# Kernel optimization log

Hardware: AMD Instinct MI355X
Metric: run time of the kernel (lower is better)

Reference implementation:

```python
import jax, jax.numpy as jnp
import numpy as np

G, NPG, MAXN = 1024, 40, 51   # graphs, nodes/graph, dense pad size
EPG = 80                       # edges per graph
N, E = G * NPG, G * EPG
D_IN, D_OUT, D_EDGE = 64, 32, 16


def _lin(key, fan_in, shape):
    b = 1.0 / np.sqrt(fan_in)
    return jax.random.uniform(key, shape, jnp.float32, -b, b)


def setup_inputs() -> dict:
    key = jax.random.key(0)
    ks = jax.random.split(key, 24)
    node_features = jax.random.randint(ks[0], (N, 9), 0, 128)
    edge_features = jax.random.randint(ks[1], (E, 3), 0, 8)
    offs = jnp.repeat(jnp.arange(G) * NPG, EPG)
    src = jax.random.randint(ks[2], (E,), 0, NPG) + offs
    dst = jax.random.randint(ks[3], (E,), 0, NPG) + offs
    edge_index = jnp.stack([src, dst])
    batch = jnp.repeat(jnp.arange(G), NPG)
    inp = dict(node_features=node_features, edge_features=edge_features,
               edge_index=edge_index, batch=batch)
    # OGB-style encoders: one embedding table per feature column, summed
    inp['atom_emb'] = jax.random.normal(ks[4], (9, 128, D_IN), jnp.float32) * 0.1
    inp['bond_emb'] = jax.random.normal(ks[5], (3, 8, D_EDGE), jnp.float32) * 0.1
    # edge-conditioned weight MLP: 16 -> 1024 -> 256 -> 64*32 (no bias)
    inp['gW1'] = _lin(ks[6], 16, (16, 1024))
    inp['gW2'] = _lin(ks[7], 1024, (1024, 256))
    inp['gW3'] = _lin(ks[8], 256, (256, D_IN * D_OUT))
    # NNConv root weight + bias
    inp['root'] = _lin(ks[9], D_IN, (D_IN, D_OUT))
    inp['conv_bias'] = jnp.zeros((D_OUT,), jnp.float32)
    # readout MLP: 51*32 -> 256 -> 128 -> 32 -> 8 -> 1
    dims = [MAXN * D_OUT, 256, 128, 32, 8, 1]
    for i in range(5):
        inp[f'mW{i+1}'] = _lin(ks[10 + 2 * i], dims[i], (dims[i], dims[i + 1]))
        inp[f'mb{i+1}'] = _lin(ks[11 + 2 * i], dims[i], (dims[i + 1],))
    return inp


def reference(node_features, edge_features, edge_index, batch,
              atom_emb, bond_emb, gW1, gW2, gW3, root, conv_bias,
              mW1, mb1, mW2, mb2, mW3, mb3, mW4, mb4, mW5, mb5):
    # encoders: sum of per-column embeddings
    x = jnp.sum(atom_emb[jnp.arange(9), node_features], axis=1)      # [N,64]
    e = jnp.sum(bond_emb[jnp.arange(3), edge_features], axis=1)      # [E,16]
    # per-edge weight matrix via MLP
    h = jax.nn.relu(e @ gW1)
    h = jax.nn.relu(h @ gW2)
    w = (h @ gW3).reshape(-1, D_IN, D_OUT)                           # [E,64,32]
    # NNConv: gather src, per-edge matmul, scatter-add to dst, + root + bias
    src, dst = edge_index[0], edge_index[1]
    msg = jnp.einsum('ed,edo->eo', x[src], w)                        # [E,32]
    agg = jax.ops.segment_sum(msg, dst, num_segments=N)              # [N,32]
    out = agg + x @ root + conv_bias
    # to_dense_batch(max_num_nodes=51); exactly NPG nodes per graph, zero-pad
    dense = jnp.zeros((G, MAXN, D_OUT), out.dtype).at[:, :NPG].set(
        out.reshape(G, NPG, D_OUT))
    f = dense.reshape(G, MAXN * D_OUT)                               # [G,1632]
    f = jax.nn.relu(f @ mW1 + mb1)
    f = jax.nn.relu(f @ mW2 + mb2)
    f = jax.nn.relu(f @ mW3 + mb3)
    f = jax.nn.relu(f @ mW4 + mb4)
    return f @ mW5 + mb5                                             # [G,1]
```

## Files before the change

### kernel.cpp

```cpp
#include <hip/hip_runtime.h>

#define NNODES 40960
#define NEDGES 81920
#define NG     1024
#define NCOMBO 512

__global__ void k_atom(const int* __restrict__ nf, const float* __restrict__ emb,
                       float* __restrict__ x) {
    int gid = blockIdx.x * blockDim.x + threadIdx.x;
    int n = gid >> 6, d = gid & 63;
    const int* nfr = nf + n * 9;
    float acc = 0.f;
#pragma unroll
    for (int c = 0; c < 9; ++c) {
        int idx = nfr[c];
        acc += emb[((c << 7) + idx) * 64 + d];
    }
    x[gid] = acc;
}

__global__ void k_rootinit(const float* __restrict__ x, const float* __restrict__ root,
                           const float* __restrict__ bias, float* __restrict__ out) {
    int gid = blockIdx.x * blockDim.x + threadIdx.x;
    int n = gid >> 5, o = gid & 31;
    const float* xr = x + n * 64;
    float acc = bias[o];
#pragma unroll
    for (int d = 0; d < 64; ++d) acc += xr[d] * root[d * 32 + o];
    out[gid] = acc;
}

__global__ void k_cid(const int* __restrict__ ef, int* __restrict__ cid) {
    int e = blockIdx.x * blockDim.x + threadIdx.x;
    if (e < NEDGES)
        cid[e] = (ef[e * 3] << 6) | (ef[e * 3 + 1] << 3) | ef[e * 3 + 2];
}

__global__ void k_etab(const float* __restrict__ bemb, float* __restrict__ etab) {
    int gid = blockIdx.x * blockDim.x + threadIdx.x;
    int c = gid >> 4, j = gid & 15;
    int f0 = c >> 6, f1 = (c >> 3) & 7, f2 = c & 7;
    etab[gid] = bemb[(0 * 8 + f0) * 16 + j] + bemb[(1 * 8 + f1) * 16 + j] +
                bemb[(2 * 8 + f2) * 16 + j];
}

__global__ void k_gemm_naive(const float* __restrict__ A, const float* __restrict__ B,
                             const float* __restrict__ bias, float* __restrict__ C,
                             int M, int N, int K, int relu) {
    int gid = blockIdx.x * blockDim.x + threadIdx.x;
    if (gid >= M * N) return;
    int m = gid / N, n = gid - m * N;
    const float* a = A + m * K;
    float acc = bias ? bias[n] : 0.f;
    for (int k = 0; k < K; ++k) acc += a[k] * B[k * N + n];
    if (relu) acc = fmaxf(acc, 0.f);
    C[gid] = acc;
}

template <int BM, int BN, int BK, int TM, int TN>
__global__ __launch_bounds__(256)
void k_gemm_tiled(const float* __restrict__ A, const float* __restrict__ B,
                  const float* __restrict__ bias, float* __restrict__ C,
                  float* __restrict__ Cp, int M, int N, int K, int KS, int relu) {
    constexpr int TX = BN / TN;
    constexpr int TY = BM / TM;
    static_assert(TX * TY == 256, "block must be 256 threads");
    __shared__ float As[BK][BM + 4];
    __shared__ float Bs[BK][BN + 4];
    const int tx = threadIdx.x % TX, ty = threadIdx.x / TX;
    const int row0 = blockIdx.y * BM, col0 = blockIdx.x * BN;
    const int z = blockIdx.z;
    const int k_begin = z * KS, k_end = k_begin + KS;

    const int am = threadIdx.x >> 2;
    const int ak = (threadIdx.x & 3) << 2;
    const int bk = threadIdx.x >> 4;
    const int bn = (threadIdx.x & 15) << 2;

    float acc[TM][TN] = {};
    for (int k0 = k_begin; k0 < k_end; k0 += BK) {
        float4 av = *reinterpret_cast<const float4*>(&A[(row0 + am) * K + k0 + ak]);
        float4 bv = *reinterpret_cast<const float4*>(&B[(k0 + bk) * N + col0 + bn]);
        As[ak + 0][am] = av.x;
        As[ak + 1][am] = av.y;
        As[ak + 2][am] = av.z;
        As[ak + 3][am] = av.w;
        *reinterpret_cast<float4*>(&Bs[bk][bn]) = bv;
        __syncthreads();
#pragma unroll
        for (int k = 0; k < BK; ++k) {
            float a[TM], b[TN];
            *reinterpret_cast<float4*>(a) =
                *reinterpret_cast<const float4*>(&As[k][ty * TM]);
            *reinterpret_cast<float4*>(b) =
                *reinterpret_cast<const float4*>(&Bs[k][tx * TN]);
#pragma unroll
            for (int i = 0; i < TM; ++i)
#pragma unroll
                for (int j = 0; j < TN; ++j) acc[i][j] += a[i] * b[j];
        }
        __syncthreads();
    }

    const int MN = M * N;
    if (gridDim.z == 1) {
#pragma unroll
        for (int i = 0; i < TM; ++i) {
            int r = row0 + ty * TM + i;
            float4 v;
            v.x = acc[i][0]; v.y = acc[i][1]; v.z = acc[i][2]; v.w = acc[i][3];
            int c = col0 + tx * TN;
            if (bias) { v.x += bias[c]; v.y += bias[c+1]; v.z += bias[c+2]; v.w += bias[c+3]; }
            if (relu) { v.x = fmaxf(v.x,0.f); v.y = fmaxf(v.y,0.f);
                        v.z = fmaxf(v.z,0.f); v.w = fmaxf(v.w,0.f); }
            *reinterpret_cast<float4*>(&C[r * N + c]) = v;
        }
    } else {
        float* dstp = Cp + z * MN;
#pragma unroll
        for (int i = 0; i < TM; ++i) {
            int r = row0 + ty * TM + i;
            float4 v;
            v.x = acc[i][0]; v.y = acc[i][1]; v.z = acc[i][2]; v.w = acc[i][3];
            *reinterpret_cast<float4*>(&dstp[r * N + col0 + tx * TN]) = v;
        }
    }
}

__global__ void k_reduceK(const float* __restrict__ Cp, const float* __restrict__ bias,
                          float* __restrict__ C, int MN, int N, int nz, int relu) {
    int i4 = (blockIdx.x * 256 + threadIdx.x) * 4;
    if (i4 >= MN) return;
    float4 acc = *reinterpret_cast<const float4*>(&Cp[i4]);
    for (int z = 1; z < nz; ++z) {
        float4 t = *reinterpret_cast<const float4*>(&Cp[z * MN + i4]);
        acc.x += t.x; acc.y += t.y; acc.z += t.z; acc.w += t.w;
    }
    if (bias) {
        int c = i4 % N;
        acc.x += bias[c]; acc.y += bias[c + 1]; acc.z += bias[c + 2]; acc.w += bias[c + 3];
    }
    if (relu) {
        acc.x = fmaxf(acc.x, 0.f); acc.y = fmaxf(acc.y, 0.f);
        acc.z = fmaxf(acc.z, 0.f); acc.w = fmaxf(acc.w, 0.f);
    }
    *reinterpret_cast<float4*>(&C[i4]) = acc;
}

__global__ void k_msg(const float* __restrict__ x, const float* __restrict__ wtab,
                      const int* __restrict__ cid, const int* __restrict__ src,
                      const int* __restrict__ dst, float* __restrict__ out) {
    int gid = blockIdx.x * blockDim.x + threadIdx.x;
    int e = gid >> 5, o = gid & 31;
    int s = src[e], d = dst[e], c = cid[e];
    const float* xr = x + s * 64;
    const float* w = wtab + c * 2048 + o;
    float acc = 0.f;
#pragma unroll
    for (int k = 0; k < 64; ++k) acc += xr[k] * w[k * 32];
    atomicAdd(&out[d * 32 + o], acc);
}

__global__ __launch_bounds__(256) void k_tail(
    const float* __restrict__ f2,
    const float* __restrict__ mW3, const float* __restrict__ mb3,
    const float* __restrict__ mW4, const float* __restrict__ mb4,
    const float* __restrict__ mW5, const float* __restrict__ mb5,
    float* __restrict__ outv) {
    __shared__ float s2[4][128];
    __shared__ float s3[4][32];
    __shared__ float s4[4][8];
    const int w = threadIdx.x >> 6, lane = threadIdx.x & 63;
    const int g = blockIdx.x * 4 + w;
    s2[w][lane] = f2[g * 128 + lane];
    s2[w][64 + lane] = f2[g * 128 + 64 + lane];
    __syncthreads();
    if (lane < 32) {
        float acc = mb3[lane];
#pragma unroll 8
        for (int k = 0; k < 128; ++k) acc += s2[w][k] * mW3[k * 32 + lane];
        s3[w][lane] = fmaxf(acc, 0.f);
    }
    __syncthreads();
    if (lane < 8) {
        float acc = mb4[lane];
#pragma unroll
        for (int k = 0; k < 32; ++k) acc += s3[w][k] * mW4[k * 8 + lane];
        s4[w][lane] = fmaxf(acc, 0.f);
    }
    __syncthreads();
    if (lane == 0) {
        float acc = mb5[0];
#pragma unroll
        for (int k = 0; k < 8; ++k) acc += s4[w][k] * mW5[k];
        outv[g] = acc;
    }
}

extern "C" void kernel_launch(void* const* d_in, const int* in_sizes, int n_in,
                              void* d_out, int out_size, void* d_ws, size_t ws_size,
                              hipStream_t stream) {
    const int*   nf      = (const int*)d_in[0];
    const int*   ef      = (const int*)d_in[1];
    const int*   eidx    = (const int*)d_in[2];
    const float* atom_emb= (const float*)d_in[4];
    const float* bond_emb= (const float*)d_in[5];
    const float* gW1     = (const float*)d_in[6];
    const float* gW2     = (const float*)d_in[7];
    const float* gW3     = (const float*)d_in[8];
    const float* root    = (const float*)d_in[9];
    const float* cbias   = (const float*)d_in[10];
    const float* mW1     = (const float*)d_in[11];
    const float* mb1     = (const float*)d_in[12];
    const float* mW2     = (const float*)d_in[13];
    const float* mb2     = (const float*)d_in[14];
    const float* mW3     = (const float*)d_in[15];
    const float* mb3     = (const float*)d_in[16];
    const float* mW4     = (const float*)d_in[17];
    const float* mb4     = (const float*)d_in[18];
    const float* mW5     = (const float*)d_in[19];
    const float* mb5     = (const float*)d_in[20];

    const int* src = eidx;
    const int* dst = eidx + NEDGES;

    float* ws = (float*)d_ws;
    float* x    = ws;
    float* out  = x + 2621440;
    float* etab = out + 1310720;
    float* h1   = etab + 8192;
    float* h2   = h1 + 524288;
    float* wtab = h2 + 131072;
    float* f1   = wtab + 1048576;
    float* f2   = f1 + 262144;
    float* part = f2 + 131072;
    int*   cid  = (int*)(part + 2097152);

    k_atom<<<NNODES * 64 / 256, 256, 0, stream>>>(nf, atom_emb, x);
    k_rootinit<<<NNODES * 32 / 256, 256, 0, stream>>>(x, root, cbias, out);
    k_cid<<<(NEDGES + 255) / 256, 256, 0, stream>>>(ef, cid);
    k_etab<<<NCOMBO * 16 / 256, 256, 0, stream>>>(bond_emb, etab);
    k_gemm_naive<<<NCOMBO * 1024 / 256, 256, 0, stream>>>(etab, gW1, nullptr, h1,
                                                          NCOMBO, 1024, 16, 1);
    k_gemm_tiled<64, 64, 16, 4, 4><<<dim3(4, 8, 16), 256, 0, stream>>>(
        h1, gW2, nullptr, nullptr, part, NCOMBO, 256, 1024, 64, 0);
    k_reduceK<<<131072 / 1024, 256, 0, stream>>>(part, nullptr, h2, 131072, 256, 16, 1);
    k_gemm_tiled<64, 64, 16, 4, 4><<<dim3(32, 8, 2), 256, 0, stream>>>(
        h2, gW3, nullptr, nullptr, part, NCOMBO, 2048, 256, 128, 0);
    k_reduceK<<<1048576 / 1024, 256, 0, stream>>>(part, nullptr, wtab, 1048576, 2048, 2, 0);
    k_msg<<<NEDGES * 32 / 256, 256, 0, stream>>>(x, wtab, cid, src, dst, out);
    k_gemm_tiled<64, 64, 16, 4, 4><<<dim3(4, 16, 8), 256, 0, stream>>>(
        out, mW1, nullptr, nullptr, part, NG, 256, 1280, 160, 0);
    k_reduceK<<<262144 / 1024, 256, 0, stream>>>(part, mb1, f1, 262144, 256, 8, 1);
    k_gemm_tiled<64, 64, 16, 4, 4><<<dim3(2, 16, 4), 256, 0, stream>>>(
        f1, mW2, nullptr, nullptr, part, NG, 128, 256, 64, 0);
    k_reduceK<<<131072 / 1024, 256, 0, stream>>>(part, mb2, f2, 131072, 128, 4, 1);
    k_tail<<<NG / 4, 256, 0, stream>>>(f2, mW3, mb3, mW4, mb4, mW5, mb5, (float*)d_out);
}
```

Baseline: 235.7 us.

## Bucket edges by bond combo so message kernel reuses weights in registers

```diff
diff --git a/kernel.cpp b/kernel.cpp
--- a/kernel.cpp
+++ b/kernel.cpp
@@ -5,43 +5,84 @@
 #define NG     1024
 #define NCOMBO 512
 
-__global__ void k_atom(const int* __restrict__ nf, const float* __restrict__ emb,
-                       float* __restrict__ x) {
-    int gid = blockIdx.x * blockDim.x + threadIdx.x;
-    int n = gid >> 6, d = gid & 63;
-    const int* nfr = nf + n * 9;
-    float acc = 0.f;
-#pragma unroll
-    for (int c = 0; c < 9; ++c) {
-        int idx = nfr[c];
-        acc += emb[((c << 7) + idx) * 64 + d];
-    }
-    x[gid] = acc;
-}
-
-__global__ void k_rootinit(const float* __restrict__ x, const float* __restrict__ root,
-                           const float* __restrict__ bias, float* __restrict__ out) {
-    int gid = blockIdx.x * blockDim.x + threadIdx.x;
-    int n = gid >> 5, o = gid & 31;
-    const float* xr = x + n * 64;
-    float acc = bias[o];
-#pragma unroll
-    for (int d = 0; d < 64; ++d) acc += xr[d] * root[d * 32 + o];
-    out[gid] = acc;
-}
-
-__global__ void k_cid(const int* __restrict__ ef, int* __restrict__ cid) {
-    int e = blockIdx.x * blockDim.x + threadIdx.x;
-    if (e < NEDGES)
-        cid[e] = (ef[e * 3] << 6) | (ef[e * 3 + 1] << 3) | ef[e * 3 + 2];
-}
-
-__global__ void k_etab(const float* __restrict__ bemb, float* __restrict__ etab) {
+__global__ void k_etab(const float* __restrict__ bemb, float* __restrict__ etab,
+                       int* __restrict__ cnt) {
     int gid = blockIdx.x * blockDim.x + threadIdx.x;
     int c = gid >> 4, j = gid & 15;
     int f0 = c >> 6, f1 = (c >> 3) & 7, f2 = c & 7;
     etab[gid] = bemb[(0 * 8 + f0) * 16 + j] + bemb[(1 * 8 + f1) * 16 + j] +
                 bemb[(2 * 8 + f2) * 16 + j];
+    if ((gid & 15) == 0) cnt[c] = 0;
+}
+
+__global__ void k_hist(const int* __restrict__ ef, int* __restrict__ cid,
+                       int* __restrict__ cnt) {
+    int e = blockIdx.x * blockDim.x + threadIdx.x;
+    if (e >= NEDGES) return;
+    int c = (ef[e * 3] << 6) | (ef[e * 3 + 1] << 3) | ef[e * 3 + 2];
+    cid[e] = c;
+    atomicAdd(&cnt[c], 1);
+}
+
+__global__ void k_scan(const int* __restrict__ cnt, int* __restrict__ bstart,
+                       int* __restrict__ bfill) {
+    __shared__ int s[NCOMBO];
+    int t = threadIdx.x;
+    int my = cnt[t];
+    s[t] = my;
+    __syncthreads();
+    for (int off = 1; off < NCOMBO; off <<= 1) {
+        int v = (t >= off) ? s[t - off] : 0;
+        __syncthreads();
+        s[t] += v;
+        __syncthreads();
+    }
+    int excl = s[t] - my;
+    bstart[t] = excl;
+    bfill[t] = excl;
+    if (t == NCOMBO - 1) bstart[NCOMBO] = NEDGES;
+}
+
+__global__ void k_scatter(const int* __restrict__ cid, const int* __restrict__ src,
+                          const int* __restrict__ dst, int* __restrict__ bfill,
+                          int2* __restrict__ ebuf) {
+    int e = blockIdx.x * blockDim.x + threadIdx.x;
+    if (e >= NEDGES) return;
+    int pos = atomicAdd(&bfill[cid[e]], 1);
+    ebuf[pos] = make_int2(src[e], dst[e]);
+}
+
+__global__ __launch_bounds__(256) void k_node(
+    const int* __restrict__ nf, const float* __restrict__ emb,
+    const float* __restrict__ root, const float* __restrict__ bias,
+    float* __restrict__ x, float* __restrict__ out) {
+    __shared__ float xs[4][64];
+    int t = threadIdx.x;
+    int nn = t >> 6, d = t & 63;
+    int n = blockIdx.x * 4 + nn;
+    const int* nfr = nf + n * 9;
+    float acc = 0.f;
+#pragma unroll
+    for (int c = 0; c < 9; ++c) {
+        int idx = nfr[c];
+        acc += emb[((c << 7) + idx) * 64 + d];
+    }
+    x[n * 64 + d] = acc;
+    xs[nn][d] = acc;
+    __syncthreads();
+    int o = t & 31, h = (t >> 5) & 1;
+    float s = h ? 0.f : bias[o];
+    int k0 = h * 32;
+#pragma unroll
+    for (int kq = 0; kq < 8; ++kq) {
+        float4 xv = *reinterpret_cast<const float4*>(&xs[nn][k0 + kq * 4]);
+        s += xv.x * root[(k0 + kq * 4 + 0) * 32 + o];
+        s += xv.y * root[(k0 + kq * 4 + 1) * 32 + o];
+        s += xv.z * root[(k0 + kq * 4 + 2) * 32 + o];
+        s += xv.w * root[(k0 + kq * 4 + 3) * 32 + o];
+    }
+    s += __shfl_xor(s, 32);
+    if (!h) out[n * 32 + o] = s;
 }
 
 __global__ void k_gemm_naive(const float* __restrict__ A, const float* __restrict__ B,
@@ -147,18 +188,43 @@
     *reinterpret_cast<float4*>(&C[i4]) = acc;
 }
 
-__global__ void k_msg(const float* __restrict__ x, const float* __restrict__ wtab,
-                      const int* __restrict__ cid, const int* __restrict__ src,
-                      const int* __restrict__ dst, float* __restrict__ out) {
-    int gid = blockIdx.x * blockDim.x + threadIdx.x;
-    int e = gid >> 5, o = gid & 31;
-    int s = src[e], d = dst[e], c = cid[e];
-    const float* xr = x + s * 64;
-    const float* w = wtab + c * 2048 + o;
-    float acc = 0.f;
-#pragma unroll
-    for (int k = 0; k < 64; ++k) acc += xr[k] * w[k * 32];
-    atomicAdd(&out[d * 32 + o], acc);
+__global__ __launch_bounds__(256) void k_msg2(
+    const float* __restrict__ x, const float* __restrict__ wtab,
+    const int* __restrict__ bstart, const int2* __restrict__ ebuf,
+    float* __restrict__ out) {
+    __shared__ float xs[64][64];
+    __shared__ int2 es[64];
+    const int t = threadIdx.x;
+    const int c = blockIdx.y;
+    const int beg = bstart[c], cnt = bstart[c + 1] - beg;
+    if (cnt == 0) return;
+    const int o = t & 31;
+    float W[64];
+    const float* wp = wtab + (c << 11) + o;
+#pragma unroll
+    for (int k = 0; k < 64; ++k) W[k] = wp[k << 5];
+
+    for (int chunk = blockIdx.x * 64; chunk < cnt; chunk += gridDim.x * 64) {
+        int nE = min(64, cnt - chunk);
+        if (t < nE) es[t] = ebuf[beg + chunk + t];
+        __syncthreads();
+        for (int i = t; i < nE * 64; i += 256) {
+            int r = i >> 6, d = i & 63;
+            xs[r][d] = x[es[r].x * 64 + d];
+        }
+        __syncthreads();
+        for (int e = t >> 5; e < nE; e += 8) {
+            float acc = 0.f;
+#pragma unroll
+            for (int kq = 0; kq < 16; ++kq) {
+                float4 xv = *reinterpret_cast<const float4*>(&xs[e][kq * 4]);
+                acc += xv.x * W[kq * 4 + 0] + xv.y * W[kq * 4 + 1] +
+                       xv.z * W[kq * 4 + 2] + xv.w * W[kq * 4 + 3];
+            }
+            atomicAdd(&out[es[e].y * 32 + o], acc);
+        }
+        __syncthreads();
+    }
 }
 
 __global__ __launch_bounds__(256) void k_tail(
@@ -234,12 +300,17 @@
     float* f1   = wtab + 1048576;
     float* f2   = f1 + 262144;
     float* part = f2 + 131072;
-    int*   cid  = (int*)(part + 2097152);
-
-    k_atom<<<NNODES * 64 / 256, 256, 0, stream>>>(nf, atom_emb, x);
-    k_rootinit<<<NNODES * 32 / 256, 256, 0, stream>>>(x, root, cbias, out);
-    k_cid<<<(NEDGES + 255) / 256, 256, 0, stream>>>(ef, cid);
-    k_etab<<<NCOMBO * 16 / 256, 256, 0, stream>>>(bond_emb, etab);
+    int*   cnt    = (int*)(part + 2097152);
+    int*   bstart = cnt + 512;
+    int*   bfill  = bstart + 513;
+    int*   cid    = bfill + 512;
+    int2*  ebuf   = (int2*)f1;
+
+    k_etab<<<NCOMBO * 16 / 256, 256, 0, stream>>>(bond_emb, etab, cnt);
+    k_hist<<<NEDGES / 256, 256, 0, stream>>>(ef, cid, cnt);
+    k_scan<<<1, NCOMBO, 0, stream>>>(cnt, bstart, bfill);
+    k_scatter<<<NEDGES / 256, 256, 0, stream>>>(cid, src, dst, bfill, ebuf);
+    k_node<<<NNODES / 4, 256, 0, stream>>>(nf, atom_emb, root, cbias, x, out);
     k_gemm_naive<<<NCOMBO * 1024 / 256, 256, 0, stream>>>(etab, gW1, nullptr, h1,
                                                           NCOMBO, 1024, 16, 1);
     k_gemm_tiled<64, 64, 16, 4, 4><<<dim3(4, 8, 16), 256, 0, stream>>>(
@@ -248,7 +319,7 @@
     k_gemm_tiled<64, 64, 16, 4, 4><<<dim3(32, 8, 2), 256, 0, stream>>>(
         h2, gW3, nullptr, nullptr, part, NCOMBO, 2048, 256, 128, 0);
     k_reduceK<<<1048576 / 1024, 256, 0, stream>>>(part, nullptr, wtab, 1048576, 2048, 2, 0);
-    k_msg<<<NEDGES * 32 / 256, 256, 0, stream>>>(x, wtab, cid, src, dst, out);
+    k_msg2<<<dim3(3, NCOMBO), 256, 0, stream>>>(x, wtab, bstart, ebuf, out);
     k_gemm_tiled<64, 64, 16, 4, 4><<<dim3(4, 16, 8), 256, 0, stream>>>(
         out, mW1, nullptr, nullptr, part, NG, 256, 1280, 160, 0);
     k_reduceK<<<262144 / 1024, 256, 0, stream>>>(part, mb1, f1, 262144, 256, 8, 1);
```

After: 258.0 us. +9.5%, slower.
